# Kernel optimization log

Measured on AMD Instinct MI355X. Metric: run time of the kernel, lower is better.

Reference implementation:

```python
import jax, jax.numpy as jnp
import numpy as np

N = 50000
IN_CH = 128
HID = 32
HEADS = 4
OUT_CH = 64
NEG_SLOPE = 0.2


def glorot(key, shape):
    fan = shape[0] + shape[-1] if len(shape) > 1 else shape[0]
    s = jnp.sqrt(6.0 / fan)
    return jax.random.uniform(key, shape, jnp.float32, -s, s)


def setup_inputs() -> dict:
    key = jax.random.key(0)
    ks = jax.random.split(key, 10)
    x = jax.random.normal(ks[0], (N, IN_CH), jnp.float32)
    edge_index = jax.random.randint(ks[1], (2, 800000), 0, N, jnp.int32)
    return {
        "x": x,
        "edge_index": edge_index,
        # layer 1 (heads=4, concat)
        "W1": glorot(ks[2], (IN_CH, HEADS * HID)),
        "att_src1": glorot(ks[3], (HEADS, HID)),
        "att_dst1": glorot(ks[4], (HEADS, HID)),
        "b1": jnp.zeros((HEADS * HID,), jnp.float32),
        # layer 2 (heads=1, no concat)
        "W2": glorot(ks[5], (HEADS * HID, OUT_CH)),
        "att_src2": glorot(ks[6], (1, OUT_CH)),
        "att_dst2": glorot(ks[7], (1, OUT_CH)),
        "b2": jnp.zeros((OUT_CH,), jnp.float32),
    }


def gat_conv(x, src, dst, W, att_src, att_dst, b, heads, out_ch, concat):
    n = x.shape[0]
    h = (x @ W).reshape(n, heads, out_ch)                  # [N,H,C]
    a_s = jnp.einsum("nhc,hc->nh", h, att_src)            # [N,H]
    a_d = jnp.einsum("nhc,hc->nh", h, att_dst)            # [N,H]
    e = jax.nn.leaky_relu(a_s[src] + a_d[dst], NEG_SLOPE)  # [E,H]
    # segment softmax over incoming edges of each destination node
    m = jax.ops.segment_max(e, dst, num_segments=n)
    ex = jnp.exp(e - m[dst])
    denom = jax.ops.segment_sum(ex, dst, num_segments=n)
    alpha = ex / (denom[dst] + 1e-16)                      # [E,H]
    msg = h[src] * alpha[:, :, None]                       # [E,H,C]
    out = jax.ops.segment_sum(msg, dst, num_segments=n)    # [N,H,C]
    out = out.reshape(n, heads * out_ch) if concat else out.mean(axis=1)
    return out + b


def _forward(x, edge_index, W1, att_src1, att_dst1, b1, W2, att_src2, att_dst2, b2):
    n = x.shape[0]
    loop = jnp.arange(n, dtype=edge_index.dtype)
    src = jnp.concatenate([edge_index[0], loop])  # PyG adds self-loops
    dst = jnp.concatenate([edge_index[1], loop])
    h = gat_conv(x, src, dst, W1, att_src1, att_dst1, b1, HEADS, HID, True)
    h = jax.nn.relu(h)
    return gat_conv(h, src, dst, W2, att_src2, att_dst2, b2, 1, OUT_CH, False)


def reference(x, edge_index, W1, att_src1, att_dst1, b1, W2, att_src2, att_dst2, b2):
    return _forward(x, edge_index, W1, att_src1, att_dst1, b1, W2, att_src2, att_dst2, b2)
```

## Files before the change

### kernel.cpp

```cpp
#include <hip/hip_runtime.h>

#define NEG_SLOPE 0.2f

typedef unsigned int uint32;
typedef unsigned short ushort;
typedef unsigned long long u64;
typedef __fp16 f16x2 __attribute__((ext_vector_type(2)));
typedef __fp16 half8 __attribute__((ext_vector_type(8)));
typedef float f32x4 __attribute__((ext_vector_type(4)));

constexpr int IN_CH = 128;
constexpr int HID = 32;
constexpr int HEADS = 4;
constexpr int OUT_CH = 64;
constexpr int C1 = HEADS * HID;
constexpr int RB = 1024;

__device__ inline uint32 pk_f16(float lo, float hi) {
    f16x2 h = __builtin_amdgcn_cvt_pkrtz(lo, hi);
    uint32 r;
    __builtin_memcpy(&r, &h, 4);
    return r;
}
__device__ inline float f16_lo(uint32 v) {
    f16x2 h;
    __builtin_memcpy(&h, &v, 4);
    return (float)h[0];
}
__device__ inline float f16_hi(uint32 v) {
    f16x2 h;
    __builtin_memcpy(&h, &v, 4);
    return (float)h[1];
}
__device__ inline float leaky(float e) {
    return fmaxf(e, 0.f) + NEG_SLOPE * fminf(e, 0.f);
}


__global__ __launch_bounds__(256) void pack_histA_kernel(const int* __restrict__ ei, int E,
                                                         uint32* __restrict__ packed,
                                                         int* __restrict__ ghist, int nblocks) {
    __shared__ int lh[256];
    int t = threadIdx.x;
    lh[t] = 0;
    __syncthreads();
    int base0 = blockIdx.x * RB;
#pragma unroll
    for (int j = 0; j < 4; j++) {
        int e = base0 + j * 256 + t;
        if (e < E) {
            uint32 s = (uint32)ei[e], d = (uint32)ei[E + e];
            uint32 v = (d << 16) | s;
            packed[e] = v;
            atomicAdd(&lh[(v >> 16) & 0xff], 1);
        }
    }
    __syncthreads();
    ghist[t * nblocks + blockIdx.x] = lh[t];
}

template <int SHIFT>
__global__ __launch_bounds__(256) void radix_hist_kernel(const uint32* __restrict__ in, int E,
                                                         int* __restrict__ ghist, int nblocks) {
    __shared__ int lh[256];
    int t = threadIdx.x;
    lh[t] = 0;
    __syncthreads();
    int base0 = blockIdx.x * RB;
#pragma unroll
    for (int j = 0; j < 4; j++) {
        int e = base0 + j * 256 + t;
        if (e < E) atomicAdd(&lh[(in[e] >> SHIFT) & 0xff], 1);
    }
    __syncthreads();
    ghist[t * nblocks + blockIdx.x] = lh[t];
}

__global__ __launch_bounds__(256) void gscanA_kernel(int* __restrict__ a, int* __restrict__ bsums,
                                                     int L) {
    __shared__ int tsum[256];
    int t = threadIdx.x;
    int base = blockIdx.x * 2048 + t * 8;
    int v[8];
    int s = 0;
#pragma unroll
    for (int i = 0; i < 8; i++) {
        v[i] = (base + i < L) ? a[base + i] : 0;
        s += v[i];
    }
    tsum[t] = s;
    __syncthreads();
    for (int d = 1; d < 256; d <<= 1) {
        int x = (t >= d) ? tsum[t - d] : 0;
        __syncthreads();
        tsum[t] += x;
        __syncthreads();
    }
    int ex = (t > 0) ? tsum[t - 1] : 0;
    if (t == 255) bsums[blockIdx.x] = tsum[255];
#pragma unroll
    for (int i = 0; i < 8; i++) {
        if (base + i < L) a[base + i] = ex;
        ex += v[i];
    }
}

__global__ void gscanB_kernel(int* __restrict__ bsums, int nb) {
    int lane = threadIdx.x;
    int v0 = (lane < nb) ? bsums[lane] : 0;
    int v1 = (64 + lane < nb) ? bsums[64 + lane] : 0;
    int s0 = v0;
#pragma unroll
    for (int d = 1; d < 64; d <<= 1) {
        int o = __shfl_up(s0, d);
        if (lane >= d) s0 += o;
    }
    int tot0 = __shfl(s0, 63);
    int s1 = v1;
#pragma unroll
    for (int d = 1; d < 64; d <<= 1) {
        int o = __shfl_up(s1, d);
        if (lane >= d) s1 += o;
    }
    s1 += tot0;
    if (lane < nb) bsums[lane] = s0 - v0;
    if (64 + lane < nb) bsums[64 + lane] = s1 - v1;
}

__global__ void gscanC_kernel(int* __restrict__ a, const int* __restrict__ bsums, int L) {
    int i = blockIdx.x * blockDim.x + threadIdx.x;
    if (i < L) a[i] += bsums[i / 2048];
}

template <int SHIFT>
__global__ __launch_bounds__(256) void radix_scatter_kernel(const uint32* __restrict__ in,
                                                            uint32* __restrict__ out,
                                                            const int* __restrict__ gbase, int E,
                                                            int nblocks) {
    __shared__ int wcnt[4][256];
    __shared__ int bbase[256];
    int t = threadIdx.x, w = t >> 6, lane = t & 63;
    wcnt[0][t] = 0;
    wcnt[1][t] = 0;
    wcnt[2][t] = 0;
    wcnt[3][t] = 0;
    bbase[t] = gbase[t * nblocks + blockIdx.x];
    __syncthreads();
    int base0 = blockIdx.x * RB;
    uint32 vals[4];
    int buck[4], prank[4];
    bool valid[4];
#pragma unroll
    for (int j = 0; j < 4; j++) {
        int e = base0 + w * 256 + j * 64 + lane;
        valid[j] = e < E;
        uint32 v = valid[j] ? in[e] : 0xffffffffu;
        vals[j] = v;
        int b = (v >> SHIFT) & 0xff;
        buck[j] = b;
        u64 mask = ~0ULL;
#pragma unroll
        for (int bit = 0; bit < 8; bit++) {
            bool p = (b >> bit) & 1;
            u64 bal = __ballot(p);
            mask &= p ? bal : ~bal;
        }
        u64 below = mask & ((1ULL << lane) - 1ULL);
        int pr = __popcll(below);
        int leaderLane = __ffsll((long long)mask) - 1;
        int prior = 0;
        if (lane == leaderLane) {
            prior = wcnt[w][b];
            wcnt[w][b] = prior + __popcll(mask);
        }
        prior = __shfl(prior, leaderLane);
        prank[j] = prior + pr;
    }
    __syncthreads();
    {
        int b = t;
        int acc = bbase[b];
#pragma unroll
        for (int w2 = 0; w2 < 4; w2++) {
            int x = wcnt[w2][b];
            wcnt[w2][b] = acc;
            acc += x;
        }
    }
    __syncthreads();
#pragma unroll
    for (int j = 0; j < 4; j++)
        if (valid[j]) out[wcnt[w][buck[j]] + prank[j]] = vals[j];
}

__global__ void offsets_bsearch_kernel(const uint32* __restrict__ sorted, int E,
                                       int* __restrict__ offsets, int N) {
    int n = blockIdx.x * blockDim.x + threadIdx.x;
    if (n > N) return;
    int lo = 0, hi = E;
    while (lo < hi) {
        int mid = (lo + hi) >> 1;
        uint32 d = sorted[mid] >> 16;
        if (d < (uint32)n)
            lo = mid + 1;
        else
            hi = mid;
    }
    offsets[n] = lo;
}


template <int K, int COLS, int H, bool AF16>
__global__ __launch_bounds__(256) void gemm_dots_kernel(
    const float* __restrict__ A, const float* __restrict__ W,
    const float* __restrict__ att_s, const float* __restrict__ att_d,
    uint32* __restrict__ hb, float* __restrict__ as_, float* __restrict__ ad_, int N) {
    static_assert(K == 128, "");
    constexpr int CF = COLS / 16;
    __shared__ ushort xs[64][136];
    __shared__ ushort wt[COLS][136];
    int tid = threadIdx.x;
    int row0 = blockIdx.x * 64;

#pragma unroll
    for (int l = 0; l < 4; l++) {
        int idx = tid + l * 256;
        int row = idx >> 4, kc = idx & 15;
        uint4 pkv = make_uint4(0, 0, 0, 0);
        if (row0 + row < N) {
            if constexpr (AF16) {
                pkv = *(const uint4*)((const uint32*)A + (size_t)(row0 + row) * (K / 2) + kc * 4);
            } else {
                const float* ap = A + (size_t)(row0 + row) * K + kc * 8;
                float4 v0 = *(const float4*)ap;
                float4 v1 = *(const float4*)(ap + 4);
                pkv = make_uint4(pk_f16(v0.x, v0.y), pk_f16(v0.z, v0.w), pk_f16(v1.x, v1.y),
                                 pk_f16(v1.z, v1.w));
            }
        }
        *(uint4*)&xs[row][kc * 8] = pkv;
    }
    constexpr int NP = (K / 2) * COLS / 256;
#pragma unroll
    for (int l = 0; l < NP; l++) {
        int p = tid + l * 256;
        int col = p % COLS, kp = p / COLS;
        float v0 = W[(size_t)(2 * kp) * COLS + col];
        float v1 = W[(size_t)(2 * kp + 1) * COLS + col];
        *(uint32*)&wt[col][kp * 2] = pk_f16(v0, v1);
    }
    __syncthreads();

    int w = tid >> 6, l = tid & 63;
    int q = l & 15, g = l >> 4;

    half8 af[4];
#pragma unroll
    for (int ks = 0; ks < 4; ks++) af[ks] = *(const half8*)&xs[w * 16 + q][ks * 32 + g * 8];

    f32x4 accs[CF];
#pragma unroll
    for (int cf = 0; cf < CF; cf++) {
        f32x4 a = {0.f, 0.f, 0.f, 0.f};
#pragma unroll
        for (int ks = 0; ks < 4; ks++) {
            half8 bf = *(const half8*)&wt[cf * 16 + q][ks * 32 + g * 8];
            a = __builtin_amdgcn_mfma_f32_16x16x32_f16(af[ks], bf, a, 0, 0, 0);
        }
        accs[cf] = a;
    }

    float asf[CF], adf[CF];
#pragma unroll
    for (int cf = 0; cf < CF; cf++) {
        asf[cf] = att_s[cf * 16 + q];
        adf[cf] = att_d[cf * 16 + q];
    }

#pragma unroll
    for (int r = 0; r < 4; r++) {
        int n_r = row0 + w * 16 + g * 4 + r;
        uint32 dw[CF];
        float p0 = 0.f, p1 = 0.f, p2 = 0.f, p3 = 0.f;
        float d0 = 0.f, d1 = 0.f, d2 = 0.f, d3 = 0.f;
#pragma unroll
        for (int cf = 0; cf < CF; cf++) {
            float v = accs[cf][r];
            float nb = __shfl_xor(v, 1);
            float ev = (q & 1) ? nb : v;
            float ov = (q & 1) ? v : nb;
            dw[cf] = pk_f16(ev, ov);
            float cs = v * asf[cf], cd = v * adf[cf];
            if constexpr (H == 4) {
                if (cf < 2) {
                    p0 += cs;
                    d0 += cd;
                } else if (cf < 4) {
                    p1 += cs;
                    d1 += cd;
                } else if (cf < 6) {
                    p2 += cs;
                    d2 += cd;
                } else {
                    p3 += cs;
                    d3 += cd;
                }
            } else {
                p0 += cs;
                d0 += cd;
            }
        }
#pragma unroll
        for (int dd = 1; dd < 16; dd <<= 1) {
            p0 += __shfl_xor(p0, dd);
            d0 += __shfl_xor(d0, dd);
            if constexpr (H == 4) {
                p1 += __shfl_xor(p1, dd);
                d1 += __shfl_xor(d1, dd);
                p2 += __shfl_xor(p2, dd);
                d2 += __shfl_xor(d2, dd);
                p3 += __shfl_xor(p3, dd);
                d3 += __shfl_xor(d3, dd);
            }
        }
        if (n_r < N) {
            if ((q & 1) == 0) {
                uint32* hp = hb + (size_t)n_r * (COLS / 2) + (q >> 1);
#pragma unroll
                for (int cf = 0; cf < CF; cf++) hp[cf * 8] = dw[cf];
            }
            if constexpr (H == 4) {
                if ((q >> 2) == r) {
                    int hh = q & 3;
                    float vs = hh == 0 ? p0 : hh == 1 ? p1 : hh == 2 ? p2 : p3;
                    float vd = hh == 0 ? d0 : hh == 1 ? d1 : hh == 2 ? d2 : d3;
                    as_[(size_t)n_r * 4 + hh] = vs;
                    ad_[(size_t)n_r * 4 + hh] = vd;
                }
            } else {
                if (q == r) {
                    as_[n_r] = p0;
                    ad_[n_r] = d0;
                }
            }
        }
    }
}


template <int C, int H, bool RELU, bool OUTF16>
__global__ __launch_bounds__(256) void aggregate_kernel(
    const uint32* __restrict__ hb, const float* __restrict__ as_,
    const float* __restrict__ ad_, const int* __restrict__ offsets,
    const uint32* __restrict__ csr, const float* __restrict__ bias, void* __restrict__ outp,
    int N) {
    __shared__ float plds[4][64 * H];
    __shared__ int slds[4][64];
    int gid = blockIdx.x * blockDim.x + threadIdx.x;
    int n = gid >> 6;
    int lane = threadIdx.x & 63;
    int wslot = threadIdx.x >> 6;
    if (n >= N) return;
    int off = offsets[n];
    int deg = offsets[n + 1] - off;

    float ad[H], s[H];
#pragma unroll
    for (int h = 0; h < H; h++) {
        ad[h] = ad_[(size_t)n * H + h];
        s[h] = 0.f;
    }

    constexpr int G = C / 8;
    constexpr int EPI = 64 / G;
    int eg = lane / G;
    int cl = lane % G;
    int hsel = (H == 4) ? (cl >> 2) : 0;
    float acc[8];
#pragma unroll
    for (int j = 0; j < 8; j++) acc[j] = 0.f;

    for (int base = 0; base <= deg; base += 64) {
        int my = base + lane;
        int cnt = min(64, deg + 1 - base);
        if (my <= deg) {
            int si = (my < deg) ? (int)(csr[off + my] & 0xffffu) : n;
            slds[wslot][lane] = si;
            if constexpr (H == 4) {
                float4 a = ((const float4*)as_)[si];
                float q0 = __expf(fminf(leaky(a.x + ad[0]), 80.f));
                float q1 = __expf(fminf(leaky(a.y + ad[1]), 80.f));
                float q2 = __expf(fminf(leaky(a.z + ad[2]), 80.f));
                float q3 = __expf(fminf(leaky(a.w + ad[3]), 80.f));
                s[0] += q0;
                s[1] += q1;
                s[2] += q2;
                s[3] += q3;
                ((float4*)plds[wslot])[lane] = make_float4(q0, q1, q2, q3);
            } else {
                float p = __expf(fminf(leaky(as_[si] + ad[0]), 80.f));
                s[0] += p;
                plds[wslot][lane] = p;
            }
        }
        int t2 = 0;
        for (; t2 + 2 * EPI <= cnt; t2 += 2 * EPI) {
            int tA = t2 + eg, tB = t2 + EPI + eg;
            int srcA = slds[wslot][tA];
            int srcB = slds[wslot][tB];
            float alA = plds[wslot][tA * H + hsel];
            float alB = plds[wslot][tB * H + hsel];
            uint4 uA = *(const uint4*)(hb + (size_t)srcA * (C / 2) + cl * 4);
            uint4 uB = *(const uint4*)(hb + (size_t)srcB * (C / 2) + cl * 4);
            acc[0] = fmaf(alA, f16_lo(uA.x), acc[0]);
            acc[1] = fmaf(alA, f16_hi(uA.x), acc[1]);
            acc[2] = fmaf(alA, f16_lo(uA.y), acc[2]);
            acc[3] = fmaf(alA, f16_hi(uA.y), acc[3]);
            acc[4] = fmaf(alA, f16_lo(uA.z), acc[4]);
            acc[5] = fmaf(alA, f16_hi(uA.z), acc[5]);
            acc[6] = fmaf(alA, f16_lo(uA.w), acc[6]);
            acc[7] = fmaf(alA, f16_hi(uA.w), acc[7]);
            acc[0] = fmaf(alB, f16_lo(uB.x), acc[0]);
            acc[1] = fmaf(alB, f16_hi(uB.x), acc[1]);
            acc[2] = fmaf(alB, f16_lo(uB.y), acc[2]);
            acc[3] = fmaf(alB, f16_hi(uB.y), acc[3]);
            acc[4] = fmaf(alB, f16_lo(uB.z), acc[4]);
            acc[5] = fmaf(alB, f16_hi(uB.z), acc[5]);
            acc[6] = fmaf(alB, f16_lo(uB.w), acc[6]);
            acc[7] = fmaf(alB, f16_hi(uB.w), acc[7]);
        }
        for (; t2 < cnt; t2 += EPI) {
            int te = t2 + eg;
            bool valid = te < cnt;
            int tc = valid ? te : 0;
            int src = slds[wslot][tc];
            float al = plds[wslot][tc * H + hsel];
            al = valid ? al : 0.f;
            uint4 u = *(const uint4*)(hb + (size_t)src * (C / 2) + cl * 4);
            acc[0] = fmaf(al, f16_lo(u.x), acc[0]);
            acc[1] = fmaf(al, f16_hi(u.x), acc[1]);
            acc[2] = fmaf(al, f16_lo(u.y), acc[2]);
            acc[3] = fmaf(al, f16_hi(u.y), acc[3]);
            acc[4] = fmaf(al, f16_lo(u.z), acc[4]);
            acc[5] = fmaf(al, f16_hi(u.z), acc[5]);
            acc[6] = fmaf(al, f16_lo(u.w), acc[6]);
            acc[7] = fmaf(al, f16_hi(u.w), acc[7]);
        }
    }

#pragma unroll
    for (int d = 1; d < 64; d <<= 1)
#pragma unroll
        for (int h = 0; h < H; h++) s[h] += __shfl_xor(s[h], d);
#pragma unroll
    for (int d = G; d < 64; d <<= 1)
#pragma unroll
        for (int j = 0; j < 8; j++) acc[j] += __shfl_xor(acc[j], d);

    if (eg == 0) {
        float inv = 1.f / s[hsel];
        int c = cl * 8;
        float o[8];
#pragma unroll
        for (int j = 0; j < 8; j++) {
            o[j] = fmaf(acc[j], inv, bias[c + j]);
            if (RELU) o[j] = fmaxf(o[j], 0.f);
        }
        if constexpr (OUTF16) {
            uint4 pkv = make_uint4(pk_f16(o[0], o[1]), pk_f16(o[2], o[3]), pk_f16(o[4], o[5]),
                                   pk_f16(o[6], o[7]));
            *(uint4*)((uint32*)outp + (size_t)n * (C / 2) + cl * 4) = pkv;
        } else {
            float* out = (float*)outp;
            *(float4*)(out + (size_t)n * C + c) = make_float4(o[0], o[1], o[2], o[3]);
            *(float4*)(out + (size_t)n * C + c + 4) = make_float4(o[4], o[5], o[6], o[7]);
        }
    }
}


extern "C" void kernel_launch(void* const* d_in, const int* in_sizes, int n_in,
                              void* d_out, int out_size, void* d_ws, size_t ws_size,
                              hipStream_t stream) {
    const float* x = (const float*)d_in[0];
    const int* ei = (const int*)d_in[1];
    const float* W1 = (const float*)d_in[2];
    const float* att_src1 = (const float*)d_in[3];
    const float* att_dst1 = (const float*)d_in[4];
    const float* b1 = (const float*)d_in[5];
    const float* W2 = (const float*)d_in[6];
    const float* att_src2 = (const float*)d_in[7];
    const float* att_dst2 = (const float*)d_in[8];
    const float* b2 = (const float*)d_in[9];

    int N = in_sizes[0] / IN_CH;
    int E = in_sizes[1] / 2;

    char* wsp = (char*)d_ws;
    size_t off = 0;
    auto carve = [&](size_t bytes) -> void* {
        void* p = wsp + off;
        off = (off + bytes + 255) & ~(size_t)255;
        return p;
    };
    int nblocks = (E + RB - 1) / RB;
    int L = 256 * nblocks;
    int nsb = (L + 2047) / 2048;

    uint32* packed = (uint32*)carve((size_t)E * 4);
    uint32* tmp = (uint32*)carve((size_t)E * 4);
    int* ghist = (int*)carve((size_t)L * 4);
    int* bsums = (int*)carve(4096);
    int* offsets = (int*)carve((size_t)(N + 1) * 4);
    uint32* h1b = (uint32*)carve((size_t)N * C1 * 2);
    uint32* h2b = (uint32*)carve((size_t)N * OUT_CH * 2);
    uint32* out1h = (uint32*)carve((size_t)N * C1 * 2);
    float* as1 = (float*)carve((size_t)N * HEADS * 4);
    float* ad1 = (float*)carve((size_t)N * HEADS * 4);
    float* as2 = (float*)carve((size_t)N * 4);
    float* ad2 = (float*)carve((size_t)N * 4);

    pack_histA_kernel<<<nblocks, 256, 0, stream>>>(ei, E, packed, ghist, nblocks);
    gscanA_kernel<<<nsb, 256, 0, stream>>>(ghist, bsums, L);
    gscanB_kernel<<<1, 64, 0, stream>>>(bsums, nsb);
    gscanC_kernel<<<(L + 255) / 256, 256, 0, stream>>>(ghist, bsums, L);
    radix_scatter_kernel<16><<<nblocks, 256, 0, stream>>>(packed, tmp, ghist, E, nblocks);
    radix_hist_kernel<24><<<nblocks, 256, 0, stream>>>(tmp, E, ghist, nblocks);
    gscanA_kernel<<<nsb, 256, 0, stream>>>(ghist, bsums, L);
    gscanB_kernel<<<1, 64, 0, stream>>>(bsums, nsb);
    gscanC_kernel<<<(L + 255) / 256, 256, 0, stream>>>(ghist, bsums, L);
    radix_scatter_kernel<24><<<nblocks, 256, 0, stream>>>(tmp, packed, ghist, E, nblocks);
    offsets_bsearch_kernel<<<(N + 256) / 256, 256, 0, stream>>>(packed, E, offsets, N);

    int nwaveblocks = (N * 64 + 255) / 256;
    int ngemmblocks = (N + 63) / 64;

    gemm_dots_kernel<128, 128, 4, false>
        <<<ngemmblocks, 256, 0, stream>>>(x, W1, att_src1, att_dst1, h1b, as1, ad1, N);
    aggregate_kernel<128, 4, true, true>
        <<<nwaveblocks, 256, 0, stream>>>(h1b, as1, ad1, offsets, packed, b1, (void*)out1h, N);

    gemm_dots_kernel<128, 64, 1, true><<<ngemmblocks, 256, 0, stream>>>(
        (const float*)out1h, W2, att_src2, att_dst2, h2b, as2, ad2, N);
    aggregate_kernel<64, 1, false, false>
        <<<nwaveblocks, 256, 0, stream>>>(h2b, as2, ad2, offsets, packed, b2, d_out, N);
}
```

Measured before the change: 148.4 us.

## Replace two-pass LSD radix sort with MSD bucket scatter plus per-bucket local sort

```diff
diff --git a/kernel.cpp b/kernel.cpp
--- a/kernel.cpp
+++ b/kernel.cpp
@@ -37,9 +37,9 @@
 }
 
 
-__global__ __launch_bounds__(256) void pack_histA_kernel(const int* __restrict__ ei, int E,
-                                                         uint32* __restrict__ packed,
-                                                         int* __restrict__ ghist, int nblocks) {
+__global__ __launch_bounds__(256) void pack_hist_kernel(const int* __restrict__ ei, int E,
+                                                        uint32* __restrict__ packed,
+                                                        int* __restrict__ ghist, int nblocks) {
     __shared__ int lh[256];
     int t = threadIdx.x;
     lh[t] = 0;
@@ -52,28 +52,11 @@
             uint32 s = (uint32)ei[e], d = (uint32)ei[E + e];
             uint32 v = (d << 16) | s;
             packed[e] = v;
-            atomicAdd(&lh[(v >> 16) & 0xff], 1);
-        }
-    }
-    __syncthreads();
-    ghist[t * nblocks + blockIdx.x] = lh[t];
-}
-
-template <int SHIFT>
-__global__ __launch_bounds__(256) void radix_hist_kernel(const uint32* __restrict__ in, int E,
-                                                         int* __restrict__ ghist, int nblocks) {
-    __shared__ int lh[256];
-    int t = threadIdx.x;
-    lh[t] = 0;
-    __syncthreads();
-    int base0 = blockIdx.x * RB;
-#pragma unroll
-    for (int j = 0; j < 4; j++) {
-        int e = base0 + j * 256 + t;
-        if (e < E) atomicAdd(&lh[(in[e] >> SHIFT) & 0xff], 1);
-    }
-    __syncthreads();
-    ghist[t * nblocks + blockIdx.x] = lh[t];
+            atomicAdd(&lh[v >> 24], 1);
+        }
+    }
+    __syncthreads();
+    ghist[(size_t)t * nblocks + blockIdx.x] = lh[t];
 }
 
 __global__ __launch_bounds__(256) void gscanA_kernel(int* __restrict__ a, int* __restrict__ bsums,
@@ -132,81 +115,60 @@
     if (i < L) a[i] += bsums[i / 2048];
 }
 
-template <int SHIFT>
-__global__ __launch_bounds__(256) void radix_scatter_kernel(const uint32* __restrict__ in,
-                                                            uint32* __restrict__ out,
-                                                            const int* __restrict__ gbase, int E,
-                                                            int nblocks) {
-    __shared__ int wcnt[4][256];
-    __shared__ int bbase[256];
-    int t = threadIdx.x, w = t >> 6, lane = t & 63;
-    wcnt[0][t] = 0;
-    wcnt[1][t] = 0;
-    wcnt[2][t] = 0;
-    wcnt[3][t] = 0;
-    bbase[t] = gbase[t * nblocks + blockIdx.x];
+__global__ __launch_bounds__(256) void scatter_msd_kernel(const uint32* __restrict__ in,
+                                                          uint32* __restrict__ out,
+                                                          const int* __restrict__ gbase, int E,
+                                                          int nblocks) {
+    __shared__ int lbase[256];
+    int t = threadIdx.x;
+    lbase[t] = gbase[(size_t)t * nblocks + blockIdx.x];
     __syncthreads();
     int base0 = blockIdx.x * RB;
-    uint32 vals[4];
-    int buck[4], prank[4];
-    bool valid[4];
 #pragma unroll
     for (int j = 0; j < 4; j++) {
-        int e = base0 + w * 256 + j * 64 + lane;
-        valid[j] = e < E;
-        uint32 v = valid[j] ? in[e] : 0xffffffffu;
-        vals[j] = v;
-        int b = (v >> SHIFT) & 0xff;
-        buck[j] = b;
-        u64 mask = ~0ULL;
-#pragma unroll
-        for (int bit = 0; bit < 8; bit++) {
-            bool p = (b >> bit) & 1;
-            u64 bal = __ballot(p);
-            mask &= p ? bal : ~bal;
-        }
-        u64 below = mask & ((1ULL << lane) - 1ULL);
-        int pr = __popcll(below);
-        int leaderLane = __ffsll((long long)mask) - 1;
-        int prior = 0;
-        if (lane == leaderLane) {
-            prior = wcnt[w][b];
-            wcnt[w][b] = prior + __popcll(mask);
-        }
-        prior = __shfl(prior, leaderLane);
-        prank[j] = prior + pr;
-    }
-    __syncthreads();
-    {
-        int b = t;
-        int acc = bbase[b];
-#pragma unroll
-        for (int w2 = 0; w2 < 4; w2++) {
-            int x = wcnt[w2][b];
-            wcnt[w2][b] = acc;
-            acc += x;
-        }
-    }
-    __syncthreads();
-#pragma unroll
-    for (int j = 0; j < 4; j++)
-        if (valid[j]) out[wcnt[w][buck[j]] + prank[j]] = vals[j];
-}
-
-__global__ void offsets_bsearch_kernel(const uint32* __restrict__ sorted, int E,
-                                       int* __restrict__ offsets, int N) {
-    int n = blockIdx.x * blockDim.x + threadIdx.x;
-    if (n > N) return;
-    int lo = 0, hi = E;
-    while (lo < hi) {
-        int mid = (lo + hi) >> 1;
-        uint32 d = sorted[mid] >> 16;
-        if (d < (uint32)n)
-            lo = mid + 1;
-        else
-            hi = mid;
-    }
-    offsets[n] = lo;
+        int e = base0 + j * 256 + t;
+        if (e < E) {
+            uint32 v = in[e];
+            int slot = atomicAdd(&lbase[v >> 24], 1);
+            out[slot] = v;
+        }
+    }
+}
+
+__global__ __launch_bounds__(256) void local_sort_kernel(const uint32* __restrict__ in,
+                                                         uint32* __restrict__ out,
+                                                         const int* __restrict__ ghist, int nblocks,
+                                                         int* __restrict__ offsets, int N, int E) {
+    __shared__ int hist[256];
+    __shared__ int cum[256];
+    int b = blockIdx.x;
+    int t = threadIdx.x;
+    int segstart = ghist[(size_t)b * nblocks];
+    int segend = (b + 1 < 256) ? ghist[(size_t)(b + 1) * nblocks] : E;
+    hist[t] = 0;
+    __syncthreads();
+    for (int i = segstart + t; i < segend; i += 256) atomicAdd(&hist[(in[i] >> 16) & 0xff], 1);
+    __syncthreads();
+    int v = hist[t];
+    cum[t] = v;
+    __syncthreads();
+    for (int d = 1; d < 256; d <<= 1) {
+        int x = (t >= d) ? cum[t - d] : 0;
+        __syncthreads();
+        cum[t] += x;
+        __syncthreads();
+    }
+    int myExcl = cum[t] - v;
+    int dstv = b * 256 + t;
+    if (dstv < N) offsets[dstv] = segstart + myExcl;
+    if (b == 0 && t == 0) offsets[N] = E;
+    hist[t] = myExcl;
+    __syncthreads();
+    for (int i = segstart + t; i < segend; i += 256) {
+        uint32 w = in[i];
+        int slot = atomicAdd(&hist[(w >> 16) & 0xff], 1);
+        out[segstart + slot] = w;
+    }
 }
 
 
@@ -520,17 +482,13 @@
     float* as2 = (float*)carve((size_t)N * 4);
     float* ad2 = (float*)carve((size_t)N * 4);
 
-    pack_histA_kernel<<<nblocks, 256, 0, stream>>>(ei, E, packed, ghist, nblocks);
+    int nbuckets = (N + 255) / 256;
+    pack_hist_kernel<<<nblocks, 256, 0, stream>>>(ei, E, packed, ghist, nblocks);
     gscanA_kernel<<<nsb, 256, 0, stream>>>(ghist, bsums, L);
     gscanB_kernel<<<1, 64, 0, stream>>>(bsums, nsb);
     gscanC_kernel<<<(L + 255) / 256, 256, 0, stream>>>(ghist, bsums, L);
-    radix_scatter_kernel<16><<<nblocks, 256, 0, stream>>>(packed, tmp, ghist, E, nblocks);
-    radix_hist_kernel<24><<<nblocks, 256, 0, stream>>>(tmp, E, ghist, nblocks);
-    gscanA_kernel<<<nsb, 256, 0, stream>>>(ghist, bsums, L);
-    gscanB_kernel<<<1, 64, 0, stream>>>(bsums, nsb);
-    gscanC_kernel<<<(L + 255) / 256, 256, 0, stream>>>(ghist, bsums, L);
-    radix_scatter_kernel<24><<<nblocks, 256, 0, stream>>>(tmp, packed, ghist, E, nblocks);
-    offsets_bsearch_kernel<<<(N + 256) / 256, 256, 0, stream>>>(packed, E, offsets, N);
+    scatter_msd_kernel<<<nblocks, 256, 0, stream>>>(packed, tmp, ghist, E, nblocks);
+    local_sort_kernel<<<nbuckets, 256, 0, stream>>>(tmp, packed, ghist, nblocks, offsets, N, E);
 
     int nwaveblocks = (N * 64 + 255) / 256;
     int ngemmblocks = (N + 63) / 64;
```

Result: faster. 129.2 us (median of 2 runs) (-12.9%).
